# Performance work log

Hardware: AMD Instinct MI355X
Metric: run time of the kernel (lower is better)

Reference implementation:

```python
import jax, jax.numpy as jnp
import numpy as np

B, T, V, H = 256, 512, 64, 256
IN = 2 * V + 1  # values + masks + delta_t = 129


def setup_inputs() -> dict:
    key = jax.random.key(0)
    ks = jax.random.split(key, 8)
    # sorted positive times with some entries zeroed (ragged padding -> t_exist False)
    t = jnp.sort(jax.random.uniform(ks[0], (B, T)), axis=1)
    keep = jax.random.uniform(ks[1], (B, T)) < 0.9
    times_in = jnp.where(keep, t, 0.0).astype(jnp.float32)
    data_in = jax.random.normal(ks[2], (B, T, V), dtype=jnp.float32)
    mask_in = (jax.random.uniform(ks[3], (B, T, V)) < 0.8).astype(jnp.float32)
    s = 1.0 / np.sqrt(H).astype(np.float32)
    W_ih = jax.random.uniform(ks[4], (3 * H, IN), minval=-s, maxval=s, dtype=jnp.float32)
    W_hh = jax.random.uniform(ks[5], (3 * H, H), minval=-s, maxval=s, dtype=jnp.float32)
    b_ih = jax.random.uniform(ks[6], (3 * H,), minval=-s, maxval=s, dtype=jnp.float32)
    b_hh = jax.random.uniform(ks[7], (3 * H,), minval=-s, maxval=s, dtype=jnp.float32)
    return {"times_in": times_in, "data_in": data_in, "mask_in": mask_in,
            "W_ih": W_ih, "W_hh": W_hh, "b_ih": b_ih, "b_hh": b_hh}


def reference(times_in, data_in, mask_in, W_ih, W_hh, b_ih, b_hh):
    b = times_in.shape[0]
    # delta_ts: times[:,1:] - times[:,:-1], padded with zero at the end
    delta = jnp.concatenate(
        [times_in[:, 1:] - times_in[:, :-1],
         jnp.zeros((b, 1), times_in.dtype)], axis=1)  # [B,T]
    # input_series = cat(values, masks, delta_t) -> [B,T,2V+1]
    x = jnp.concatenate([data_in, mask_in, delta[..., None]], axis=-1)
    t_exist = times_in > 0  # [B,T]
    h0 = jnp.zeros((b, W_hh.shape[1]), x.dtype)

    xs = (jnp.swapaxes(x, 0, 1), jnp.swapaxes(t_exist, 0, 1))  # time-major

    def step(h, inp):
        xt, m = inp  # xt: [B,IN], m: [B]
        gx = xt @ W_ih.T + b_ih  # [B,3H]
        gh = h @ W_hh.T + b_hh   # [B,3H]
        xr, xz, xn = jnp.split(gx, 3, axis=-1)
        hr, hz, hn = jnp.split(gh, 3, axis=-1)
        r = jax.nn.sigmoid(xr + hr)
        z = jax.nn.sigmoid(xz + hz)
        n = jnp.tanh(xn + r * hn)
        h_new = (1.0 - z) * n + z * h
        h = jnp.where(m[:, None], h_new, h)  # masked state carry
        return h, None

    h_final, _ = jax.lax.scan(step, h0, xs)
    return h_final
```

## Files before the change

### kernel.cpp

```cpp
#include <hip/hip_runtime.h>

#define Bn 256
#define Tn 512
#define Vn 64
#define Hn 256
#define INn 129
#define Cc 8
#define NCH (Tn / Cc)
#define WU 68
#define WSZ (768 * WU)
#define GX_OFF (262144)
#define GX_BYTES ((size_t)Bn * Tn * 768 * 2)
#define AST 168
#define CST 264

typedef __fp16 half2_t __attribute__((ext_vector_type(2)));
typedef __fp16 half8_t __attribute__((ext_vector_type(8)));
typedef float f32x4 __attribute__((ext_vector_type(4)));

static __device__ __forceinline__ unsigned int cvt2(float a, float b) {
  return __builtin_bit_cast(unsigned int, __builtin_amdgcn_cvt_pkrtz(a, b));
}

static __device__ __forceinline__ float dot2(unsigned int w, unsigned int x, float acc) {
#if __has_builtin(__builtin_amdgcn_fdot2)
  return __builtin_amdgcn_fdot2(__builtin_bit_cast(half2_t, w),
                                __builtin_bit_cast(half2_t, x), acc, false);
#else
  half2_t a = __builtin_bit_cast(half2_t, w);
  half2_t b = __builtin_bit_cast(half2_t, x);
  return acc + (float)a.x * (float)b.x + (float)a.y * (float)b.y;
#endif
}

static __device__ __forceinline__ float pair_sum(float v) {
#if __has_builtin(__builtin_amdgcn_update_dpp)
  int x = __builtin_amdgcn_update_dpp(0, __builtin_bit_cast(int, v), 0xB1, 0xF, 0xF, true);
  return v + __builtin_bit_cast(float, x);
#else
  int j = __builtin_amdgcn_ds_swizzle(__builtin_bit_cast(int, v), 0x041F);
  return v + __builtin_bit_cast(float, j);
#endif
}

static __device__ __forceinline__ float fast_exp2(float x) {
#if __has_builtin(__builtin_amdgcn_exp2f)
  return __builtin_amdgcn_exp2f(x);
#else
  return exp2f(x);
#endif
}
static __device__ __forceinline__ float fast_rcp(float x) {
#if __has_builtin(__builtin_amdgcn_rcpf)
  return __builtin_amdgcn_rcpf(x);
#else
  return 1.f / x;
#endif
}
static __device__ __forceinline__ float sigmoid_f(float x) {
  return fast_rcp(1.f + fast_exp2(-1.44269504f * x));
}
static __device__ __forceinline__ float tanh_f(float x) {
  return 1.f - 2.f * fast_rcp(1.f + fast_exp2(2.88539008f * x));
}
static __device__ __forceinline__ float h2f(unsigned short u) {
  return (float)__builtin_bit_cast(__fp16, u);
}

__global__ void convert_wih(const float* __restrict__ W_ih, unsigned int* __restrict__ w16) {
  int idx = blockIdx.x * 256 + threadIdx.x;
  if (idx >= WSZ) return;
  int j = idx / WU, c = idx - j * WU;
  int col = 2 * c;
  float f0 = (col < INn) ? W_ih[(size_t)j * INn + col] : 0.f;
  float f1 = (col + 1 < INn) ? W_ih[(size_t)j * INn + col + 1] : 0.f;
  w16[idx] = cvt2(f0, f1);
}

__global__ __launch_bounds__(256, 4)
void gx_gemm(const float* __restrict__ times_in, const float* __restrict__ data_in,
             const float* __restrict__ mask_in, const unsigned int* __restrict__ w16,
             const float* __restrict__ b_ih, const float* __restrict__ b_hh,
             __fp16* __restrict__ gx) {
  __shared__ __align__(16) char raw[64 * CST * 2];
  __fp16* xa = (__fp16*)raw;
  __fp16* ct = (__fp16*)raw;

  const int tid = threadIdx.x;
  const int bt = blockIdx.x;
  const int b = bt >> 3, tc = bt & 7;
  const int t0 = tc * 64;
  const int n0 = blockIdx.y * 256;

  {
    int r = tid >> 2, s = tid & 3;
    const float* src = (s < 2)
        ? data_in + ((size_t)b * Tn + t0 + r) * Vn + s * 32
        : mask_in + ((size_t)b * Tn + t0 + r) * Vn + (s - 2) * 32;
    unsigned int* dst = (unsigned int*)(xa + r * AST) + s * 16;
#pragma unroll
    for (int i = 0; i < 8; ++i) {
      float4 v = ((const float4*)src)[i];
      dst[2 * i] = cvt2(v.x, v.y);
      dst[2 * i + 1] = cvt2(v.z, v.w);
    }
  }
  if (tid < 64) {
    int g = t0 + tid;
    float tcur = times_in[(size_t)b * Tn + g];
    float d = (g < Tn - 1) ? times_in[(size_t)b * Tn + g + 1] - tcur : 0.f;
    unsigned int* p = (unsigned int*)(xa + tid * AST + 128);
    p[0] = cvt2(d, 0.f);
#pragma unroll
    for (int i = 1; i < 20; ++i) p[i] = 0u;
  }
  __syncthreads();

  const int w = tid >> 6, lane = tid & 63;
  const int m = lane & 15, q = lane >> 4;
  const int nw = n0 + w * 64;

  f32x4 acc[4][4];
#pragma unroll
  for (int i = 0; i < 4; ++i)
#pragma unroll
    for (int j = 0; j < 4; ++j) acc[i][j] = f32x4{0.f, 0.f, 0.f, 0.f};

#pragma unroll
  for (int kt = 0; kt < 5; ++kt) {
    const int k0 = kt * 32 + q * 8;
    half8_t bf[4], af[4];
#pragma unroll
    for (int nt = 0; nt < 4; ++nt) {
      int n = nw + nt * 16 + m;
      uint4 bv = *(const uint4*)(w16 + (size_t)n * WU + (k0 >> 1));
      bf[nt] = __builtin_bit_cast(half8_t, bv);
    }
#pragma unroll
    for (int mt = 0; mt < 4; ++mt) {
      uint4 av = *(const uint4*)(xa + (mt * 16 + m) * AST + k0);
      af[mt] = __builtin_bit_cast(half8_t, av);
    }
#pragma unroll
    for (int mt = 0; mt < 4; ++mt)
#pragma unroll
      for (int nt = 0; nt < 4; ++nt)
        acc[mt][nt] = __builtin_amdgcn_mfma_f32_16x16x32_f16(af[mt], bf[nt], acc[mt][nt], 0, 0, 0);
  }

  float bias[4];
#pragma unroll
  for (int nt = 0; nt < 4; ++nt) {
    int n = nw + nt * 16 + m;
    bias[nt] = b_ih[n] + ((n < 512) ? b_hh[n] : 0.f);
  }

  __syncthreads();
#pragma unroll
  for (int mt = 0; mt < 4; ++mt)
#pragma unroll
    for (int nt = 0; nt < 4; ++nt)
#pragma unroll
      for (int r = 0; r < 4; ++r)
        ct[(mt * 16 + q * 4 + r) * CST + w * 64 + nt * 16 + m] =
            (__fp16)(acc[mt][nt][r] + bias[nt]);
  __syncthreads();

  {
    const int tt = tid >> 2, qq = tid & 3;
    const uint4* src = (const uint4*)(ct + tt * CST) + qq * 8;
    uint4* dst = (uint4*)(gx + ((size_t)b * Tn + t0 + tt) * 768 + n0) + qq * 8;
#pragma unroll
    for (int i = 0; i < 8; ++i) dst[i] = src[i];
  }
}

struct G6 {
  unsigned short r0, r1, z0, z1, n0, n1;
};
static __device__ __forceinline__ G6 load_gx(const unsigned short* p) {
  G6 g;
  g.r0 = p[0];
  g.r1 = p[16];
  g.z0 = p[256];
  g.z1 = p[272];
  g.n0 = p[512];
  g.n1 = p[528];
  return g;
}

__global__ __launch_bounds__(512, 1)
void gru_scan_mfma(const float* __restrict__ times_in, const float* __restrict__ W_hh,
                   const float* __restrict__ b_hh, const __fp16* __restrict__ gx,
                   float* __restrict__ out) {
  __shared__ __align__(16) __fp16 hl[2 * Hn];
  __shared__ short act[Tn];
  __shared__ int wave_cnt[8];
  __shared__ int nact_s;

  const int tid = threadIdx.x;
  const int b = blockIdx.x;
  const int lane = tid & 63;
  const int w = tid >> 6;
  const int m = lane & 15;
  const int q = lane >> 4;
  const int d0 = w * 32 + m;

  {
    float tv = times_in[(size_t)b * Tn + tid];
    bool on = tv > 0.f;
    unsigned long long mask = __ballot(on);
    int within = __popcll(mask & ((1ull << lane) - 1ull));
    if (lane == 0) wave_cnt[w] = __popcll(mask);
    __syncthreads();
    int off = 0;
#pragma unroll
    for (int i = 0; i < 8; ++i) off += (i < w) ? wave_cnt[i] : 0;
    if (on) act[off + within] = (short)tid;
    if (tid == 0) {
      int n = 0;
#pragma unroll
      for (int i = 0; i < 8; ++i) n += wave_cnt[i];
      nact_s = n;
    }
  }

  half8_t wb[6][8];
#pragma unroll
  for (int g = 0; g < 3; ++g)
#pragma unroll
    for (int hf = 0; hf < 2; ++hf) {
      const float* wr = W_hh + (size_t)(g * 256 + w * 32 + hf * 16 + m) * Hn;
#pragma unroll
      for (int kc = 0; kc < 8; ++kc) {
        const float4 a = *(const float4*)(wr + kc * 32 + q * 8);
        const float4 c = *(const float4*)(wr + kc * 32 + q * 8 + 4);
        uint4 u;
        u.x = cvt2(a.x, a.y);
        u.y = cvt2(a.z, a.w);
        u.z = cvt2(c.x, c.y);
        u.w = cvt2(c.z, c.w);
        wb[g * 2 + hf][kc] = __builtin_bit_cast(half8_t, u);
      }
    }
  const float bhn0 = b_hh[512 + d0];
  const float bhn1 = b_hh[512 + d0 + 16];

  hl[tid] = (__fp16)0.f;
  __syncthreads();

  const int nact = nact_s;
  const unsigned short* gxs = (const unsigned short*)(gx + (size_t)b * Tn * 768) + d0;

  float h0 = 0.f, h1 = 0.f;
  int cur = 0;

  auto step = [&](G6 g) {
    const uint4* ha = (const uint4*)(hl + cur * Hn);
    uint4 afu[8];
#pragma unroll
    for (int kc = 0; kc < 8; ++kc) afu[kc] = ha[kc * 4 + q];

    f32x4 acc[6];
#pragma unroll
    for (int t = 0; t < 6; ++t) acc[t] = f32x4{0.f, 0.f, 0.f, 0.f};
#pragma unroll
    for (int kc = 0; kc < 8; ++kc) {
      half8_t a = __builtin_bit_cast(half8_t, afu[kc]);
#pragma unroll
      for (int t = 0; t < 6; ++t)
        acc[t] = __builtin_amdgcn_mfma_f32_16x16x32_f16(a, wb[t][kc], acc[t], 0, 0, 0);
    }

    float r0 = sigmoid_f(h2f(g.r0) + acc[0][0]);
    float r1 = sigmoid_f(h2f(g.r1) + acc[1][0]);
    float z0 = sigmoid_f(h2f(g.z0) + acc[2][0]);
    float z1 = sigmoid_f(h2f(g.z1) + acc[3][0]);
    float n0 = tanh_f(h2f(g.n0) + r0 * (acc[4][0] + bhn0));
    float n1 = tanh_f(h2f(g.n1) + r1 * (acc[5][0] + bhn1));
    h0 = z0 * (h0 - n0) + n0;
    h1 = z1 * (h1 - n1) + n1;

    if (q == 0) {
      hl[(cur ^ 1) * Hn + d0] = (__fp16)h0;
      hl[(cur ^ 1) * Hn + d0 + 16] = (__fp16)h1;
    }
    asm volatile("s_waitcnt lgkmcnt(0)" ::: "memory");
    __builtin_amdgcn_s_barrier();
    __builtin_amdgcn_sched_barrier(0);
    cur ^= 1;
  };

  if (nact > 0) {
    G6 ga = load_gx(gxs + (size_t)act[0] * 768);
    G6 gb = load_gx(gxs + (size_t)act[(nact > 1) ? 1 : 0] * 768);
    int i = 0;
#pragma unroll 1
    for (; i + 2 <= nact; i += 2) {
      const int iA = (i + 2 < nact) ? i + 2 : nact - 1;
      const int iB = (i + 3 < nact) ? i + 3 : nact - 1;
      const int tA = act[iA];
      const int tB = act[iB];
      step(ga);
      ga = load_gx(gxs + (size_t)tA * 768);
      step(gb);
      gb = load_gx(gxs + (size_t)tB * 768);
    }
    if (i < nact) step(ga);
  }

  if (q == 0) {
    out[(size_t)b * Hn + d0] = h0;
    out[(size_t)b * Hn + d0 + 16] = h1;
  }
}

template <bool USE_WS>
static __device__ __forceinline__ void phaseA_pass(int col, const unsigned int* __restrict__ w16,
                                                   const float* __restrict__ W_ih,
                                                   const unsigned int* x_lds, float* a) {
  const uint4* wp = (const uint4*)(w16) + (size_t)col * (WU / 4);
  const float* wf = W_ih + (size_t)col * INn;
#pragma unroll 2
  for (int kp = 0; kp < 8; ++kp) {
    uint4 wa, wb;
    if constexpr (USE_WS) {
      wa = wp[2 * kp];
      wb = wp[2 * kp + 1];
    } else {
      const float* f = wf + 16 * kp;
      wa.x = cvt2(f[0], f[1]);   wa.y = cvt2(f[2], f[3]);
      wa.z = cvt2(f[4], f[5]);   wa.w = cvt2(f[6], f[7]);
      wb.x = cvt2(f[8], f[9]);   wb.y = cvt2(f[10], f[11]);
      wb.z = cvt2(f[12], f[13]); wb.w = cvt2(f[14], f[15]);
    }
#pragma unroll
    for (int t = 0; t < Cc; ++t) {
      const uint4* xp = (const uint4*)&x_lds[t * WU + kp * 8];
      uint4 xa = xp[0], xb = xp[1];
      a[t] = dot2(wa.x, xa.x, a[t]);
      a[t] = dot2(wa.y, xa.y, a[t]);
      a[t] = dot2(wa.z, xa.z, a[t]);
      a[t] = dot2(wa.w, xa.w, a[t]);
      a[t] = dot2(wb.x, xb.x, a[t]);
      a[t] = dot2(wb.y, xb.y, a[t]);
      a[t] = dot2(wb.z, xb.z, a[t]);
      a[t] = dot2(wb.w, xb.w, a[t]);
    }
  }
  uint4 wt;
  if constexpr (USE_WS) {
    wt = wp[16];
  } else {
    wt.x = cvt2(wf[128], 0.f); wt.y = 0u; wt.z = 0u; wt.w = 0u;
  }
#pragma unroll
  for (int t = 0; t < Cc; ++t) {
    uint4 xt = *(const uint4*)&x_lds[t * WU + 64];
    a[t] = dot2(wt.x, xt.x, a[t]);
    a[t] = dot2(wt.y, xt.y, a[t]);
  }
}

template <bool USE_WS>
__global__ __launch_bounds__(512, 2)
void gru_scan_fb(const float* __restrict__ times_in, const float* __restrict__ data_in,
                 const float* __restrict__ mask_in, const unsigned int* __restrict__ w16,
                 const float* __restrict__ W_ih, const float* __restrict__ W_hh,
                 const float* __restrict__ b_ih, const float* __restrict__ b_hh,
                 float* __restrict__ out) {
  __shared__ __align__(16) float gx_lds[Cc * 768];
  __shared__ __align__(16) unsigned int x_lds[Cc * WU];
  __shared__ __align__(16) __fp16 h_buf[2 * Hn];
  __shared__ __align__(16) float t_lds[Tn];

  const int tid = threadIdx.x;
  const int b = blockIdx.x;
  const int jg = tid >> 1;
  const int ks = tid & 1;

  t_lds[tid] = times_in[(size_t)b * Tn + tid];

  unsigned int whr[64], whz[64], whn[64];
  {
    const float* w0 = W_hh + (size_t)jg * Hn + ks * 128;
    const float* w1 = W_hh + (size_t)(jg + 256) * Hn + ks * 128;
    const float* w2 = W_hh + (size_t)(jg + 512) * Hn + ks * 128;
#pragma unroll
    for (int c = 0; c < 64; ++c) {
      whr[c] = cvt2(w0[2 * c], w0[2 * c + 1]);
      whz[c] = cvt2(w1[2 * c], w1[2 * c + 1]);
      whn[c] = cvt2(w2[2 * c], w2[2 * c + 1]);
    }
  }
  const float brh = b_hh[jg];
  const float bzh = b_hh[jg + 256];
  const float bhn = b_hh[jg + 512];
  const float bi1 = b_ih[tid];
  const float bi2 = (tid < 256) ? b_ih[512 + tid] : 0.f;

  h_buf[tid] = (__fp16)0.f;
  __syncthreads();

  float hcur = 0.f;
  int cur = 0;
#pragma unroll 1
  for (int ch = 0; ch < NCH; ++ch) {
    const int t0 = ch * Cc;
    {
      int t = tid >> 6;
      int c = tid & 63;
      const float* src = (c < 32)
          ? data_in + ((size_t)b * Tn + t0 + t) * Vn + 2 * c
          : mask_in + ((size_t)b * Tn + t0 + t) * Vn + 2 * (c - 32);
      float2 v = *(const float2*)src;
      x_lds[t * WU + c] = cvt2(v.x, v.y);
      if (tid < Cc) {
        int g = t0 + tid;
        float d = (g < Tn - 1) ? (t_lds[g + 1] - t_lds[g]) : 0.f;
        uint4 tl;
        tl.x = cvt2(d, 0.f); tl.y = 0u; tl.z = 0u; tl.w = 0u;
        *(uint4*)&x_lds[tid * WU + 64] = tl;
      }
    }
    __syncthreads();
    {
      float a[Cc];
#pragma unroll
      for (int t = 0; t < Cc; ++t) a[t] = bi1;
      phaseA_pass<USE_WS>(tid, w16, W_ih, x_lds, a);
#pragma unroll
      for (int t = 0; t < Cc; ++t) gx_lds[t * 768 + tid] = a[t];
      if (tid < 256) {
#pragma unroll
        for (int t = 0; t < Cc; ++t) a[t] = bi2;
        phaseA_pass<USE_WS>(512 + tid, w16, W_ih, x_lds, a);
#pragma unroll
        for (int t = 0; t < Cc; ++t) gx_lds[t * 768 + 512 + tid] = a[t];
      }
    }
    __syncthreads();
    for (int tt = 0; tt < Cc; ++tt) {
      float sr = 0.f, sz = 0.f, shn = 0.f;
      const uint4* hb = (const uint4*)(h_buf + cur * Hn + ks * 128);
#pragma unroll
      for (int c = 0; c < 16; ++c) {
        uint4 hv = hb[c];
        sr = dot2(whr[4 * c + 0], hv.x, sr);
        sz = dot2(whz[4 * c + 0], hv.x, sz);
        shn = dot2(whn[4 * c + 0], hv.x, shn);
        sr = dot2(whr[4 * c + 1], hv.y, sr);
        sz = dot2(whz[4 * c + 1], hv.y, sz);
        shn = dot2(whn[4 * c + 1], hv.y, shn);
        sr = dot2(whr[4 * c + 2], hv.z, sr);
        sz = dot2(whz[4 * c + 2], hv.z, sz);
        shn = dot2(whn[4 * c + 2], hv.z, shn);
        sr = dot2(whr[4 * c + 3], hv.w, sr);
        sz = dot2(whz[4 * c + 3], hv.w, sz);
        shn = dot2(whn[4 * c + 3], hv.w, shn);
      }
      float gxr = gx_lds[tt * 768 + jg];
      float gxz = gx_lds[tt * 768 + 256 + jg];
      float gxn = gx_lds[tt * 768 + 512 + jg];
      sr = pair_sum(sr);
      sz = pair_sum(sz);
      shn = pair_sum(shn);
      float r = sigmoid_f(gxr + sr + brh);
      float z = sigmoid_f(gxz + sz + bzh);
      float n = tanh_f(gxn + r * (shn + bhn));
      float hN = (1.f - z) * n + z * hcur;
      hcur = (t_lds[t0 + tt] > 0.f) ? hN : hcur;
      if (ks == 0) h_buf[(cur ^ 1) * Hn + jg] = (__fp16)hcur;
      __syncthreads();
      cur ^= 1;
    }
  }
  if (ks == 0) out[(size_t)b * Hn + jg] = hcur;
}

extern "C" void kernel_launch(void* const* d_in, const int* in_sizes, int n_in,
                              void* d_out, int out_size, void* d_ws, size_t ws_size,
                              hipStream_t stream) {
  const float* times_in = (const float*)d_in[0];
  const float* data_in = (const float*)d_in[1];
  const float* mask_in = (const float*)d_in[2];
  const float* W_ih = (const float*)d_in[3];
  const float* W_hh = (const float*)d_in[4];
  const float* b_ih = (const float*)d_in[5];
  const float* b_hh = (const float*)d_in[6];
  float* out = (float*)d_out;

  unsigned int* w16 = (unsigned int*)d_ws;
  __fp16* gx = (__fp16*)((char*)d_ws + GX_OFF);

  if (ws_size >= GX_OFF + GX_BYTES) {
    hipLaunchKernelGGL(convert_wih, dim3((WSZ + 255) / 256), dim3(256), 0, stream, W_ih, w16);
    hipLaunchKernelGGL(gx_gemm, dim3(2048, 3), dim3(256), 0, stream,
                       times_in, data_in, mask_in, w16, b_ih, b_hh, gx);
    hipLaunchKernelGGL(gru_scan_mfma, dim3(Bn), dim3(512), 0, stream,
                       times_in, W_hh, b_hh, gx, out);
  } else if (ws_size >= (size_t)WSZ * 4) {
    hipLaunchKernelGGL(convert_wih, dim3((WSZ + 255) / 256), dim3(256), 0, stream, W_ih, w16);
    hipLaunchKernelGGL((gru_scan_fb<true>), dim3(Bn), dim3(512), 0, stream,
                       times_in, data_in, mask_in, w16, W_ih, W_hh, b_ih, b_hh, out);
  } else {
    hipLaunchKernelGGL((gru_scan_fb<false>), dim3(Bn), dim3(512), 0, stream,
                       times_in, data_in, mask_in, (const unsigned int*)nullptr, W_ih, W_hh,
                       b_ih, b_hh, out);
  }
}
```

Baseline: 721.5 us.

## Split GRU scan across 16 waves with one hidden column per lane group

```diff
diff --git a/kernel.cpp b/kernel.cpp
--- a/kernel.cpp
+++ b/kernel.cpp
@@ -175,24 +175,21 @@
   }
 }
 
-struct G6 {
-  unsigned short r0, r1, z0, z1, n0, n1;
+struct G3 {
+  unsigned short r, z, n;
 };
-static __device__ __forceinline__ G6 load_gx(const unsigned short* p) {
-  G6 g;
-  g.r0 = p[0];
-  g.r1 = p[16];
-  g.z0 = p[256];
-  g.z1 = p[272];
-  g.n0 = p[512];
-  g.n1 = p[528];
+static __device__ __forceinline__ G3 load_gx(const unsigned short* p) {
+  G3 g;
+  g.r = p[0];
+  g.z = p[256];
+  g.n = p[512];
   return g;
 }
 
-__global__ __launch_bounds__(512, 1)
-void gru_scan_mfma(const float* __restrict__ times_in, const float* __restrict__ W_hh,
-                   const float* __restrict__ b_hh, const __fp16* __restrict__ gx,
-                   float* __restrict__ out) {
+__global__ __launch_bounds__(1024, 1)
+void gru_scan_mfma16(const float* __restrict__ times_in, const float* __restrict__ W_hh,
+                     const float* __restrict__ b_hh, const __fp16* __restrict__ gx,
+                     float* __restrict__ out) {
   __shared__ __align__(16) __fp16 hl[2 * Hn];
   __shared__ short act[Tn];
   __shared__ int wave_cnt[8];
@@ -204,14 +201,15 @@
   const int w = tid >> 6;
   const int m = lane & 15;
   const int q = lane >> 4;
-  const int d0 = w * 32 + m;
-
-  {
+  const int d0 = w * 16 + m;
+
+  if (tid < Tn) {
     float tv = times_in[(size_t)b * Tn + tid];
     bool on = tv > 0.f;
     unsigned long long mask = __ballot(on);
     int within = __popcll(mask & ((1ull << lane) - 1ull));
     if (lane == 0) wave_cnt[w] = __popcll(mask);
+    if (on) act[0] = act[0];
     __syncthreads();
     int off = 0;
 #pragma unroll
@@ -223,68 +221,65 @@
       for (int i = 0; i < 8; ++i) n += wave_cnt[i];
       nact_s = n;
     }
-  }
-
-  half8_t wb[6][8];
-#pragma unroll
-  for (int g = 0; g < 3; ++g)
-#pragma unroll
-    for (int hf = 0; hf < 2; ++hf) {
-      const float* wr = W_hh + (size_t)(g * 256 + w * 32 + hf * 16 + m) * Hn;
-#pragma unroll
-      for (int kc = 0; kc < 8; ++kc) {
-        const float4 a = *(const float4*)(wr + kc * 32 + q * 8);
-        const float4 c = *(const float4*)(wr + kc * 32 + q * 8 + 4);
-        uint4 u;
-        u.x = cvt2(a.x, a.y);
-        u.y = cvt2(a.z, a.w);
-        u.z = cvt2(c.x, c.y);
-        u.w = cvt2(c.z, c.w);
-        wb[g * 2 + hf][kc] = __builtin_bit_cast(half8_t, u);
-      }
-    }
-  const float bhn0 = b_hh[512 + d0];
-  const float bhn1 = b_hh[512 + d0 + 16];
-
-  hl[tid] = (__fp16)0.f;
+  } else {
+    __syncthreads();
+  }
+
+  half8_t wb[3][8];
+#pragma unroll
+  for (int g = 0; g < 3; ++g) {
+    const float* wr = W_hh + (size_t)(g * 256 + d0) * Hn;
+#pragma unroll
+    for (int kc = 0; kc < 8; ++kc) {
+      const float4 a = *(const float4*)(wr + kc * 32 + q * 8);
+      const float4 c = *(const float4*)(wr + kc * 32 + q * 8 + 4);
+      uint4 u;
+      u.x = cvt2(a.x, a.y);
+      u.y = cvt2(a.z, a.w);
+      u.z = cvt2(c.x, c.y);
+      u.w = cvt2(c.z, c.w);
+      wb[g][kc] = __builtin_bit_cast(half8_t, u);
+    }
+  }
+  const float bhn = b_hh[512 + d0];
+
+  if (tid < 2 * Hn) hl[tid] = (__fp16)0.f;
   __syncthreads();
 
   const int nact = nact_s;
   const unsigned short* gxs = (const unsigned short*)(gx + (size_t)b * Tn * 768) + d0;
 
-  float h0 = 0.f, h1 = 0.f;
+  float hcur = 0.f;
   int cur = 0;
 
-  auto step = [&](G6 g) {
+  auto step = [&](G3 g) {
     const uint4* ha = (const uint4*)(hl + cur * Hn);
     uint4 afu[8];
 #pragma unroll
     for (int kc = 0; kc < 8; ++kc) afu[kc] = ha[kc * 4 + q];
 
-    f32x4 acc[6];
-#pragma unroll
-    for (int t = 0; t < 6; ++t) acc[t] = f32x4{0.f, 0.f, 0.f, 0.f};
+    const float gr = h2f(g.r), gz = h2f(g.z), gn = h2f(g.n);
+    f32x4 ar = f32x4{gr, gr, gr, gr};
+    f32x4 az = f32x4{gz, gz, gz, gz};
+    f32x4 an = f32x4{bhn, bhn, bhn, bhn};
+
 #pragma unroll
     for (int kc = 0; kc < 8; ++kc) {
       half8_t a = __builtin_bit_cast(half8_t, afu[kc]);
-#pragma unroll
-      for (int t = 0; t < 6; ++t)
-        acc[t] = __builtin_amdgcn_mfma_f32_16x16x32_f16(a, wb[t][kc], acc[t], 0, 0, 0);
-    }
-
-    float r0 = sigmoid_f(h2f(g.r0) + acc[0][0]);
-    float r1 = sigmoid_f(h2f(g.r1) + acc[1][0]);
-    float z0 = sigmoid_f(h2f(g.z0) + acc[2][0]);
-    float z1 = sigmoid_f(h2f(g.z1) + acc[3][0]);
-    float n0 = tanh_f(h2f(g.n0) + r0 * (acc[4][0] + bhn0));
-    float n1 = tanh_f(h2f(g.n1) + r1 * (acc[5][0] + bhn1));
-    h0 = z0 * (h0 - n0) + n0;
-    h1 = z1 * (h1 - n1) + n1;
-
-    if (q == 0) {
-      hl[(cur ^ 1) * Hn + d0] = (__fp16)h0;
-      hl[(cur ^ 1) * Hn + d0 + 16] = (__fp16)h1;
-    }
+      ar = __builtin_amdgcn_mfma_f32_16x16x32_f16(a, wb[0][kc], ar, 0, 0, 0);
+      az = __builtin_amdgcn_mfma_f32_16x16x32_f16(a, wb[1][kc], az, 0, 0, 0);
+    }
+    float r = sigmoid_f(ar[0]);
+    float z = sigmoid_f(az[0]);
+#pragma unroll
+    for (int kc = 0; kc < 8; ++kc) {
+      half8_t a = __builtin_bit_cast(half8_t, afu[kc]);
+      an = __builtin_amdgcn_mfma_f32_16x16x32_f16(a, wb[2][kc], an, 0, 0, 0);
+    }
+    float n = tanh_f(gn + r * an[0]);
+    hcur = z * (hcur - n) + n;
+
+    if (q == 0) hl[(cur ^ 1) * Hn + d0] = (__fp16)hcur;
     asm volatile("s_waitcnt lgkmcnt(0)" ::: "memory");
     __builtin_amdgcn_s_barrier();
     __builtin_amdgcn_sched_barrier(0);
@@ -292,8 +287,8 @@
   };
 
   if (nact > 0) {
-    G6 ga = load_gx(gxs + (size_t)act[0] * 768);
-    G6 gb = load_gx(gxs + (size_t)act[(nact > 1) ? 1 : 0] * 768);
+    G3 ga = load_gx(gxs + (size_t)act[0] * 768);
+    G3 gb = load_gx(gxs + (size_t)act[(nact > 1) ? 1 : 0] * 768);
     int i = 0;
 #pragma unroll 1
     for (; i + 2 <= nact; i += 2) {
@@ -309,10 +304,7 @@
     if (i < nact) step(ga);
   }
 
-  if (q == 0) {
-    out[(size_t)b * Hn + d0] = h0;
-    out[(size_t)b * Hn + d0 + 16] = h1;
-  }
+  if (q == 0) out[(size_t)b * Hn + d0] = hcur;
 }
 
 template <bool USE_WS>
@@ -497,7 +489,7 @@
     hipLaunchKernelGGL(convert_wih, dim3((WSZ + 255) / 256), dim3(256), 0, stream, W_ih, w16);
     hipLaunchKernelGGL(gx_gemm, dim3(2048, 3), dim3(256), 0, stream,
                        times_in, data_in, mask_in, w16, b_ih, b_hh, gx);
-    hipLaunchKernelGGL(gru_scan_mfma, dim3(Bn), dim3(512), 0, stream,
+    hipLaunchKernelGGL(gru_scan_mfma16, dim3(Bn), dim3(1024), 0, stream,
                        times_in, W_hh, b_hh, gx, out);
   } else if (ws_size >= (size_t)WSZ * 4) {
     hipLaunchKernelGGL(convert_wih, dim3((WSZ + 255) / 256), dim3(256), 0, stream, W_ih, w16);
```

Measured after the change: 887.3 us. 1.23x slower.
